# Kernel optimization log

Hardware: AMD Instinct MI355X
Metric: run time of the kernel (lower is better)

Reference implementation:

```python
import jax, jax.numpy as jnp
import numpy as np

NS, NV = 32, 8            # scalar / vector multiplicities
N_NODES, N_EDGES = 40000, 120000
HID = 3 * NS              # edge-feature / MLP hidden size
WNUM = NS*NS + NS*NV + NV*NV + NV*NS + NV*NV  # 1664 tp weights per edge


def setup_inputs() -> dict:
    key = jax.random.key(0)
    ks = jax.random.split(key, 8)
    return {
        'node_attr': jax.random.normal(ks[0], (N_NODES, NS + 3*NV), jnp.float32),
        'edge_attr': jax.random.normal(ks[1], (N_EDGES, HID), jnp.float32),
        'edge_sh':   jax.random.normal(ks[2], (N_EDGES, 4), jnp.float32),
        'W1': jax.random.normal(ks[3], (HID, HID), jnp.float32) / np.sqrt(HID),
        'b1': jnp.zeros((HID,), jnp.float32),
        'W2': jax.random.normal(ks[4], (HID, WNUM), jnp.float32) / np.sqrt(HID),
        'b2': jnp.zeros((WNUM,), jnp.float32),
        'edge_src': jax.random.randint(ks[5], (N_EDGES,), 0, N_NODES, jnp.int32),
        'edge_dst': jax.random.randint(ks[6], (N_EDGES,), 0, N_NODES, jnp.int32),
    }


def _tp_conv(node_attr, edge_attr, edge_sh, W1, b1, W2, b2, edge_src, edge_dst):
    E = edge_attr.shape[0]
    N = node_attr.shape[0]
    # --- gather destination node features per edge ---
    x = node_attr[edge_dst]                      # [E, NS+3*NV]
    x0 = x[:, :NS]                               # [E, NS]  0e scalars
    x1 = x[:, NS:].reshape(E, NV, 3)             # [E, NV, 3]  1o vectors
    s0 = edge_sh[:, 0]                           # [E]     sh 0e
    sh1 = edge_sh[:, 1:4]                        # [E, 3]  sh 1o
    # --- per-edge weight generation MLP ---
    h = jax.nn.relu(edge_attr @ W1 + b1)
    w = h @ W2 + b2                              # [E, WNUM]
    o = 0
    w1 = w[:, o:o+NS*NS].reshape(E, NS, NS); o += NS*NS   # 0e x 0e -> 0e
    w2 = w[:, o:o+NS*NV].reshape(E, NS, NV); o += NS*NV   # 0e x 1o -> 1o
    w3 = w[:, o:o+NV*NV].reshape(E, NV, NV); o += NV*NV   # 1o x 0e -> 1o
    w4 = w[:, o:o+NV*NS].reshape(E, NV, NS); o += NV*NS   # 1o x 1o -> 0e (dot)
    w5 = w[:, o:o+NV*NV].reshape(E, NV, NV)               # 1o x 1o -> 1e (cross)
    inv_s3 = 1.0 / np.sqrt(3.0).astype(np.float32)
    inv_s2 = 1.0 / np.sqrt(2.0).astype(np.float32)
    n0 = 1.0 / np.sqrt(NS + NV).astype(np.float32)        # fan-in norm, 0e out
    n1o = n0                                              # fan-in norm, 1o out
    n1e = 1.0 / np.sqrt(NV).astype(np.float32)            # fan-in norm, 1e out
    # --- fully connected tensor product (CG contraction per path) ---
    out0 = (jnp.einsum('eu,euv->ev', x0, w1) * s0[:, None]
            + jnp.einsum('eum,em,euv->ev', x1, sh1, w4) * inv_s3) * n0   # [E, NS]
    out1o = (jnp.einsum('eu,euv->ev', x0, w2)[:, :, None] * sh1[:, None, :]
             + jnp.einsum('eum,euv->evm', x1, w3) * s0[:, None, None]) * n1o  # [E,NV,3]
    cr = jnp.cross(x1, sh1[:, None, :])                                  # [E, NV, 3]
    out1e = jnp.einsum('eum,euv->evm', cr, w5) * (inv_s2 * n1e)          # [E, NV, 3]
    tp = jnp.concatenate([out0, out1o.reshape(E, -1), out1e.reshape(E, -1)], axis=-1)
    # --- scatter-mean to source nodes ---
    seg = jax.ops.segment_sum(tp, edge_src, num_segments=N)
    cnt = jax.ops.segment_sum(jnp.ones((E,), tp.dtype), edge_src, num_segments=N)
    return seg / jnp.maximum(cnt, 1.0)[:, None]            # [N, NS+6*NV]


def reference(node_attr, edge_attr, edge_sh, W1, b1, W2, b2, edge_src, edge_dst):
    return _tp_conv(node_attr, edge_attr, edge_sh, W1, b1, W2, b2, edge_src, edge_dst)
```

## Files before the change

kernel.cpp:

```cpp
#include <hip/hip_runtime.h>
#include <hip/hip_bf16.h>

typedef short short8 __attribute__((ext_vector_type(8)));
typedef float f32x4 __attribute__((ext_vector_type(4)));
typedef unsigned int uint2v __attribute__((ext_vector_type(2)));

#define HID 96
#define WNUM 1664
#define NA_DIM 56
#define OUT_DIM 80
#define EPB 64
#define NT_TOT 104
#define CHW 208
#define NCH 8
#define NTC 13
#define APAD 104

#define N0f 0.158113883f
#define INV_S3 0.5773502692f
#define C_OUT1E 0.25f

__device__ __forceinline__ unsigned short f2bf(float x) {
  unsigned u = __builtin_bit_cast(unsigned, x);
  u += 0x7FFFu + ((u >> 16) & 1u);
  return (unsigned short)(u >> 16);
}
__device__ __forceinline__ unsigned short f2bf_hw(float x) {
  __hip_bfloat16 b = __float2bfloat16(x);
  return __builtin_bit_cast(unsigned short, b);
}

#if __has_builtin(__builtin_amdgcn_fdot2_f32_bf16)
typedef __bf16 bf16x2 __attribute__((ext_vector_type(2)));
#define DOT2(acc, w, x) \
  acc = __builtin_amdgcn_fdot2_f32_bf16(__builtin_bit_cast(bf16x2, (unsigned)(w)), \
                                        __builtin_bit_cast(bf16x2, (unsigned)(x)), (acc), false)
#else
#define DOT2(acc, w, x) do { \
  unsigned _w = (w), _x = (x); \
  acc = fmaf(__builtin_bit_cast(float, _w << 16), __builtin_bit_cast(float, _x << 16), acc); \
  acc = fmaf(__builtin_bit_cast(float, _w & 0xFFFF0000u), __builtin_bit_cast(float, _x & 0xFFFF0000u), acc); \
} while (0)
#endif

__device__ __forceinline__ int perm_col(int J) {
  int c = J / CHW, l = J - (J / CHW) * CHW;
  if (l < 128) { int vp = l >> 5, u = l & 31; return u * 32 + 4 * c + vp; }
  if (l < 160) { int u = l - 128; return 1024 + u * 8 + c; }
  if (l < 168) { int u = l - 160; return 1280 + u * 8 + c; }
  if (l < 200) { int q = l - 168; int vp = q >> 3, u = q & 7; return 1344 + u * 32 + 4 * c + vp; }
  { int u = l - 200; return 1600 + u * 8 + c; }
}

__global__ __launch_bounds__(256) void hist_kernel(
    const int* __restrict__ edge_src, int* __restrict__ hist, int E) {
  int e = blockIdx.x * 256 + threadIdx.x;
  if (e < E) atomicAdd(&hist[edge_src[e]], 1);
}

__global__ __launch_bounds__(256) void scan1_kernel(
    const int* __restrict__ hist, int* __restrict__ excl,
    int* __restrict__ bsum, int n) {
  __shared__ int s[256];
  int t = threadIdx.x, i = blockIdx.x * 256 + t;
  int v = (i < n) ? hist[i] : 0;
  s[t] = v;
  __syncthreads();
  #pragma unroll
  for (int off = 1; off < 256; off <<= 1) {
    int tv = (t >= off) ? s[t - off] : 0;
    __syncthreads();
    s[t] += tv;
    __syncthreads();
  }
  if (i < n) excl[i] = s[t] - v;
  if (t == 255) bsum[blockIdx.x] = s[255];
}

__global__ __launch_bounds__(256) void scan2_kernel(int* __restrict__ bsum, int nb) {
  __shared__ int s[256];
  int t = threadIdx.x;
  int v = (t < nb) ? bsum[t] : 0;
  s[t] = v;
  __syncthreads();
  #pragma unroll
  for (int off = 1; off < 256; off <<= 1) {
    int tv = (t >= off) ? s[t - off] : 0;
    __syncthreads();
    s[t] += tv;
    __syncthreads();
  }
  if (t < nb) bsum[t] = s[t] - v;
}

__global__ __launch_bounds__(256) void scan3_kernel(
    const int* __restrict__ excl, const int* __restrict__ bsum,
    int* __restrict__ start, int* __restrict__ cur, int n) {
  int i = blockIdx.x * 256 + threadIdx.x;
  if (i < n) {
    int v = excl[i] + bsum[blockIdx.x];
    start[i] = v;
    cur[i] = v;
  }
}

__global__ __launch_bounds__(256) void scatter_kernel(
    const int* __restrict__ edge_src, int* __restrict__ cur,
    int* __restrict__ pos, int E) {
  int e = blockIdx.x * 256 + threadIdx.x;
  if (e < E) {
    pos[e] = atomicAdd(&cur[edge_src[e]], 1);
  }
}

__global__ __launch_bounds__(256) void prep_kernel(
    const float* __restrict__ W2, const float* __restrict__ W1,
    const float* __restrict__ b2, unsigned short* __restrict__ W2p,
    unsigned short* __restrict__ W1p, float* __restrict__ b2p,
    int* __restrict__ hist, int nhist)
{
  int gid = blockIdx.x * 256 + threadIdx.x;
  if (gid < nhist) hist[gid] = 0;
  const int NW2 = NT_TOT * 3 * 64;
  const int NW1 = 18 * 64;
  if (gid < NW2) {
    int tile = gid >> 6, ln = gid & 63;
    int nt = tile / 3, s = tile - nt * 3;
    int J = nt * 16 + (ln & 15);
    int jo = perm_col(J);
    int kbase = s * 32 + ((ln >> 4) << 3);
    #pragma unroll
    for (int j = 0; j < 8; ++j)
      W2p[(size_t)gid * 8 + j] = f2bf(W2[(kbase + j) * WNUM + jo]);
  } else if (gid < NW2 + NW1) {
    int g = gid - NW2;
    int tile = g >> 6, ln = g & 63;
    int nt = tile / 3, s = tile - nt * 3;
    int col = nt * 16 + (ln & 15);
    int kbase = s * 32 + ((ln >> 4) << 3);
    #pragma unroll
    for (int j = 0; j < 8; ++j)
      W1p[(size_t)g * 8 + j] = f2bf(W1[(kbase + j) * HID + col]);
  } else if (gid < NW2 + NW1 + WNUM) {
    int J = gid - (NW2 + NW1);
    b2p[J] = b2[perm_col(J)];
  }
}

__global__ __launch_bounds__(512, 2) void fused_mfma(
    const float* __restrict__ edge_attr, const unsigned short* __restrict__ W1p,
    const float* __restrict__ b1, const unsigned short* __restrict__ W2p,
    const float* __restrict__ b2p, const float* __restrict__ node_attr,
    const float* __restrict__ edge_sh, const int* __restrict__ edge_dst,
    const int* __restrict__ pos, float* __restrict__ tpg)
{
  __shared__ __align__(16) unsigned short ws[2][EPB][212];
  __shared__ __align__(8) unsigned short x0h[EPB][32];
  __shared__ __align__(8) unsigned short x1h[EPB][3][8];
  __shared__ __align__(8) unsigned short dsuh[EPB][8];
  __shared__ __align__(8) unsigned short crsh[EPB][3][8];
  __shared__ float x1s[EPB][3][8];
  __shared__ float sh1s[EPB][3];
  __shared__ float s0s[EPB];
  __shared__ int   dsts[EPB];
  __shared__ int   poss[EPB];

  unsigned short* As = (unsigned short*)ws;
  unsigned short* hB = As + EPB * APAD;

  const int tid = threadIdx.x;
  const int e0 = blockIdx.x * EPB;

  if (tid < EPB) {
    dsts[tid] = edge_dst[e0 + tid];
    s0s[tid] = edge_sh[(size_t)(e0 + tid) * 4];
    poss[tid] = pos[e0 + tid];
  }
  if (tid >= 128 && tid < 128 + EPB * 3) {
    int i = tid - 128, e = i / 3, m = i - e * 3;
    sh1s[e][m] = edge_sh[(size_t)(e0 + e) * 4 + 1 + m];
  }
  __syncthreads();

  for (int idx = tid; idx < EPB * NA_DIM; idx += 512) {
    int e = idx / NA_DIM, c = idx - e * NA_DIM;
    float v = node_attr[(size_t)dsts[e] * NA_DIM + c];
    if (c < 32) x0h[e][c] = f2bf_hw(v);
    else { int q = c - 32; x1s[e][q % 3][q / 3] = v; x1h[e][q % 3][q / 3] = f2bf_hw(v); }
  }
  for (int idx = tid; idx < EPB * (HID / 4); idx += 512) {
    int e = idx / (HID / 4), c4 = (idx - e * (HID / 4)) * 4;
    f32x4 v = *(const f32x4*)&edge_attr[(size_t)(e0 + e) * HID + c4];
    unsigned short* d = &As[e * APAD + c4];
    d[0] = f2bf_hw(v[0]); d[1] = f2bf_hw(v[1]); d[2] = f2bf_hw(v[2]); d[3] = f2bf_hw(v[3]);
  }
  __syncthreads();

  {
    int e = tid >> 3, u = tid & 7;
    float a0 = x1s[e][0][u], a1 = x1s[e][1][u], a2 = x1s[e][2][u];
    float b0 = sh1s[e][0], b1v = sh1s[e][1], b2v = sh1s[e][2];
    dsuh[e][u] = f2bf_hw(a0 * b0 + a1 * b1v + a2 * b2v);
    crsh[e][0][u] = f2bf_hw(a1 * b2v - a2 * b1v);
    crsh[e][1][u] = f2bf_hw(a2 * b0 - a0 * b2v);
    crsh[e][2][u] = f2bf_hw(a0 * b1v - a1 * b0);
  }

  const int ln = tid & 63, wv = tid >> 6;
  const int c16 = ln & 15, q4 = (ln >> 4) << 2, k8 = (ln >> 4) << 3;

  #pragma unroll
  for (int t = 0; t < 3; ++t) {
    int tt_ = wv * 3 + t;
    int mtile = tt_ / 6, ntile = tt_ - mtile * 6;
    short8 aA[3];
    #pragma unroll
    for (int s = 0; s < 3; ++s)
      aA[s] = *(const short8*)&As[(mtile * 16 + c16) * APAD + s * 32 + k8];
    f32x4 acc = {0.f, 0.f, 0.f, 0.f};
    #pragma unroll
    for (int s = 0; s < 3; ++s) {
      short8 bfr = *(const short8*)(W1p + ((size_t)(ntile * 3 + s) * 64 + ln) * 8);
      acc = __builtin_amdgcn_mfma_f32_16x16x32_bf16(aA[s], bfr, acc, 0, 0, 0);
    }
    float bb = b1[ntile * 16 + c16];
    #pragma unroll
    for (int r = 0; r < 4; ++r)
      hB[(mtile * 16 + q4 + r) * APAD + ntile * 16 + c16] = f2bf_hw(fmaxf(acc[r] + bb, 0.f));
  }
  __syncthreads();

  short8 af[4][3];
  #pragma unroll
  for (int mt = 0; mt < 4; ++mt)
    #pragma unroll
    for (int s = 0; s < 3; ++s)
      af[mt][s] = *(const short8*)&hB[(mt * 16 + c16) * APAD + s * 32 + k8];
  __syncthreads();

  const int e = tid >> 3, tt = tid & 7;
  uint2v x0r[8], aux0, aux1;
  if (tt < 7) {
    #pragma unroll
    for (int i = 0; i < 8; ++i) x0r[i] = *(const uint2v*)&x0h[e][i * 4];
    if (tt < 4) {
      aux0 = *(const uint2v*)&dsuh[e][0];
      aux1 = *(const uint2v*)&dsuh[e][4];
    } else {
      aux0 = *(const uint2v*)&x1h[e][tt - 4][0];
      aux1 = *(const uint2v*)&x1h[e][tt - 4][4];
    }
  } else {
    #pragma unroll
    for (int m = 0; m < 3; ++m) {
      x0r[2 * m]     = *(const uint2v*)&crsh[e][m][0];
      x0r[2 * m + 1] = *(const uint2v*)&crsh[e][m][4];
    }
  }

  const int l0t = wv * 16 + c16;
  const int pc0t = (l0t & 96) | ((l0t + ((l0t >> 5) << 2)) & 31);
  const unsigned short* w2a = W2p + ((size_t)(wv * 3) * 64 + ln) * 8;
  const unsigned short* w2b = W2p + ((size_t)((wv + 8) * 3) * 64 + ln) * 8;
  const size_t CSTRIDE = (size_t)NTC * 3 * 64 * 8;
  const bool has1 = wv < (NTC - 8);

  auto compute_chunk = [&](int cc, unsigned short (*wsd)[212]) {
    const size_t cb = (size_t)cc * CSTRIDE;
    {
      f32x4 acc[4];
      #pragma unroll
      for (int mt = 0; mt < 4; ++mt) acc[mt] = (f32x4){0.f, 0.f, 0.f, 0.f};
      #pragma unroll
      for (int s = 0; s < 3; ++s) {
        short8 bfr = *(const short8*)(w2a + cb + (size_t)s * 64 * 8);
        #pragma unroll
        for (int mt = 0; mt < 4; ++mt)
          acc[mt] = __builtin_amdgcn_mfma_f32_16x16x32_bf16(af[mt][s], bfr, acc[mt], 0, 0, 0);
      }
      float bias = b2p[cc * CHW + l0t];
      #pragma unroll
      for (int mt = 0; mt < 4; ++mt)
        #pragma unroll
        for (int r = 0; r < 4; ++r)
          wsd[mt * 16 + q4 + r][pc0t] = f2bf_hw(acc[mt][r] + bias);
    }
    if (has1) {
      f32x4 acc[4];
      #pragma unroll
      for (int mt = 0; mt < 4; ++mt) acc[mt] = (f32x4){0.f, 0.f, 0.f, 0.f};
      #pragma unroll
      for (int s = 0; s < 3; ++s) {
        short8 bfr = *(const short8*)(w2b + cb + (size_t)s * 64 * 8);
        #pragma unroll
        for (int mt = 0; mt < 4; ++mt)
          acc[mt] = __builtin_amdgcn_mfma_f32_16x16x32_bf16(af[mt][s], bfr, acc[mt], 0, 0, 0);
      }
      float bias = b2p[cc * CHW + 128 + l0t];
      #pragma unroll
      for (int mt = 0; mt < 4; ++mt)
        #pragma unroll
        for (int r = 0; r < 4; ++r)
          wsd[mt * 16 + q4 + r][128 + l0t] = f2bf_hw(acc[mt][r] + bias);
    }
  };

  compute_chunk(0, ws[0]);
  __syncthreads();

  const float s0 = s0s[e];
  float* tpr = tpg + (size_t)poss[e] * OUT_DIM;

  for (int ch = 0; ch < NCH; ++ch) {
    if (ch < NCH - 1) compute_chunk(ch + 1, ws[(ch + 1) & 1]);

    const unsigned short (*wsr)[212] = ws[ch & 1];
    if (tt < 4) {
      float sa = 0.f, sb = 0.f;
      #pragma unroll
      for (int u0 = 0; u0 < 32; u0 += 8) {
        int pu  = (u0 + (tt << 2)) & 31;
        int pu2 = (u0 + 4 + (tt << 2)) & 31;
        uint2v wq  = *(const uint2v*)&wsr[e][(tt << 5) + pu];
        uint2v wq2 = *(const uint2v*)&wsr[e][(tt << 5) + pu2];
        uint2v xq  = x0r[u0 >> 2];
        uint2v xq2 = x0r[(u0 >> 2) + 1];
        DOT2(sa, wq[0], xq[0]);
        DOT2(sa, wq[1], xq[1]);
        DOT2(sb, wq2[0], xq2[0]);
        DOT2(sb, wq2[1], xq2[1]);
      }
      float s2 = 0.f;
      {
        uint2v wq  = *(const uint2v*)&wsr[e][168 + (tt << 3)];
        uint2v wq2 = *(const uint2v*)&wsr[e][168 + (tt << 3) + 4];
        DOT2(s2, wq[0], aux0[0]);
        DOT2(s2, wq[1], aux0[1]);
        DOT2(s2, wq2[0], aux1[0]);
        DOT2(s2, wq2[1], aux1[1]);
      }
      tpr[4 * ch + tt] = N0f * (s0 * (sa + sb) + INV_S3 * s2);
    } else if (tt < 7) {
      const int m = tt - 4;
      float sa = 0.f, sb = 0.f;
      #pragma unroll
      for (int u0 = 0; u0 < 32; u0 += 8) {
        uint2v wq  = *(const uint2v*)&wsr[e][128 + u0];
        uint2v wq2 = *(const uint2v*)&wsr[e][128 + u0 + 4];
        uint2v xq  = x0r[u0 >> 2];
        uint2v xq2 = x0r[(u0 >> 2) + 1];
        DOT2(sa, wq[0], xq[0]);
        DOT2(sa, wq[1], xq[1]);
        DOT2(sb, wq2[0], xq2[0]);
        DOT2(sb, wq2[1], xq2[1]);
      }
      float s2 = 0.f;
      {
        uint2v wq  = *(const uint2v*)&wsr[e][160];
        uint2v wq2 = *(const uint2v*)&wsr[e][164];
        DOT2(s2, wq[0], aux0[0]);
        DOT2(s2, wq[1], aux0[1]);
        DOT2(s2, wq2[0], aux1[0]);
        DOT2(s2, wq2[1], aux1[1]);
      }
      tpr[32 + ch * 3 + m] = N0f * (sh1s[e][m] * (sa + sb) + s0 * s2);
    } else {
      #pragma unroll
      for (int m = 0; m < 3; ++m) {
        float s2 = 0.f;
        uint2v wq  = *(const uint2v*)&wsr[e][200];
        uint2v wq2 = *(const uint2v*)&wsr[e][204];
        DOT2(s2, wq[0], x0r[2 * m][0]);
        DOT2(s2, wq[1], x0r[2 * m][1]);
        DOT2(s2, wq2[0], x0r[2 * m + 1][0]);
        DOT2(s2, wq2[1], x0r[2 * m + 1][1]);
        tpr[56 + ch * 3 + m] = C_OUT1E * s2;
      }
    }
    __syncthreads();
  }
}

__global__ __launch_bounds__(256) void gather_kernel(
    const float* __restrict__ tp, const int* __restrict__ start,
    const int* __restrict__ hist, float* __restrict__ out, int total)
{
  int idx = blockIdx.x * 256 + threadIdx.x;
  if (idx >= total) return;
  int node = idx / OUT_DIM, o = idx - node * OUT_DIM;
  int s = start[node], c = hist[node];
  float sum = 0.f;
  for (int i = 0; i < c; ++i)
    sum += tp[(size_t)(s + i) * OUT_DIM + o];
  out[idx] = sum / (float)(c > 0 ? c : 1);
}

extern "C" void kernel_launch(void* const* d_in, const int* in_sizes, int n_in,
                              void* d_out, int out_size, void* d_ws, size_t ws_size,
                              hipStream_t stream) {
  const float* node_attr = (const float*)d_in[0];
  const float* edge_attr = (const float*)d_in[1];
  const float* edge_sh   = (const float*)d_in[2];
  const float* W1        = (const float*)d_in[3];
  const float* b1        = (const float*)d_in[4];
  const float* W2        = (const float*)d_in[5];
  const float* b2        = (const float*)d_in[6];
  const int*   edge_src  = (const int*)d_in[7];
  const int*   edge_dst  = (const int*)d_in[8];
  float* out = (float*)d_out;

  const int E = in_sizes[7];
  const int N = in_sizes[0] / NA_DIM;

  char* wsb = (char*)d_ws;
  int*   hist  = (int*)(wsb + 0x000000);
  int*   excl  = (int*)(wsb + 0x040000);
  int*   start = (int*)(wsb + 0x080000);
  int*   cur   = (int*)(wsb + 0x0C0000);
  int*   bsum  = (int*)(wsb + 0x100000);
  int*   pos   = (int*)(wsb + 0x110000);
  unsigned short* W2p = (unsigned short*)(wsb + 0x200000);
  unsigned short* W1p = (unsigned short*)(wsb + 0x280000);
  float*          b2p = (float*)(wsb + 0x2C0000);
  float*          tpg = (float*)(wsb + 0x1C00000);

  const int NB = (N + 255) / 256;

  const int prep_total = NT_TOT * 3 * 64 + 18 * 64 + WNUM;
  const int prep_grid = ((prep_total > N ? prep_total : N) + 255) / 256;
  prep_kernel<<<prep_grid, 256, 0, stream>>>(W2, W1, b2, W2p, W1p, b2p, hist, N);

  hist_kernel<<<(E + 255) / 256, 256, 0, stream>>>(edge_src, hist, E);
  scan1_kernel<<<NB, 256, 0, stream>>>(hist, excl, bsum, N);
  scan2_kernel<<<1, 256, 0, stream>>>(bsum, NB);
  scan3_kernel<<<NB, 256, 0, stream>>>(excl, bsum, start, cur, N);
  scatter_kernel<<<(E + 255) / 256, 256, 0, stream>>>(edge_src, cur, pos, E);

  fused_mfma<<<E / EPB, 512, 0, stream>>>(edge_attr, W1p, b1, W2p, b2p,
                                          node_attr, edge_sh, edge_dst, pos, tpg);
  gather_kernel<<<(N * OUT_DIM + 255) / 256, 256, 0, stream>>>(
      tpg, start, hist, out, N * OUT_DIM);
}
```

Baseline: 152.6 us.

## Merge scan kernels, fold scatter into fused kernel, store per-edge results in bf16

Folds the second and third scan passes into one kernel: every block redundantly scans the block sums and adds its own offset. The separate scatter kernel goes away, and the fused MFMA kernel now claims each edge's output slot itself with an atomicAdd on the node cursor. Per-edge tensor-product outputs are stored as bf16 instead of fp32, halving the intermediate buffer traffic read by the gather kernel. The dot-product accumulators are split into more independent chains. These changes cut two launches and memory traffic at the cost of extra rounding on the intermediate values and a nondeterministic slot order.

```diff
diff --git a/kernel.cpp b/kernel.cpp
--- a/kernel.cpp
+++ b/kernel.cpp
@@ -28,6 +28,10 @@
 __device__ __forceinline__ unsigned short f2bf_hw(float x) {
   __hip_bfloat16 b = __float2bfloat16(x);
   return __builtin_bit_cast(unsigned short, b);
+}
+__device__ __forceinline__ float bf2f(unsigned short x) {
+  unsigned u = ((unsigned)x) << 16;
+  return __builtin_bit_cast(float, u);
 }
 
 #if __has_builtin(__builtin_amdgcn_fdot2_f32_bf16)
@@ -77,7 +81,9 @@
   if (t == 255) bsum[blockIdx.x] = s[255];
 }
 
-__global__ __launch_bounds__(256) void scan2_kernel(int* __restrict__ bsum, int nb) {
+__global__ __launch_bounds__(256) void scan23_kernel(
+    const int* __restrict__ excl, const int* __restrict__ bsum,
+    int* __restrict__ start, int* __restrict__ cur, int n, int nb) {
   __shared__ int s[256];
   int t = threadIdx.x;
   int v = (t < nb) ? bsum[t] : 0;
@@ -90,26 +96,12 @@
     s[t] += tv;
     __syncthreads();
   }
-  if (t < nb) bsum[t] = s[t] - v;
-}
-
-__global__ __launch_bounds__(256) void scan3_kernel(
-    const int* __restrict__ excl, const int* __restrict__ bsum,
-    int* __restrict__ start, int* __restrict__ cur, int n) {
-  int i = blockIdx.x * 256 + threadIdx.x;
+  int add = (blockIdx.x > 0) ? s[blockIdx.x - 1] : 0;
+  int i = blockIdx.x * 256 + t;
   if (i < n) {
-    int v = excl[i] + bsum[blockIdx.x];
-    start[i] = v;
-    cur[i] = v;
-  }
-}
-
-__global__ __launch_bounds__(256) void scatter_kernel(
-    const int* __restrict__ edge_src, int* __restrict__ cur,
-    int* __restrict__ pos, int E) {
-  int e = blockIdx.x * 256 + threadIdx.x;
-  if (e < E) {
-    pos[e] = atomicAdd(&cur[edge_src[e]], 1);
+    int val = excl[i] + add;
+    start[i] = val;
+    cur[i] = val;
   }
 }
 
@@ -151,8 +143,9 @@
     const float* __restrict__ edge_attr, const unsigned short* __restrict__ W1p,
     const float* __restrict__ b1, const unsigned short* __restrict__ W2p,
     const float* __restrict__ b2p, const float* __restrict__ node_attr,
-    const float* __restrict__ edge_sh, const int* __restrict__ edge_dst,
-    const int* __restrict__ pos, float* __restrict__ tpg)
+    const float* __restrict__ edge_sh, const int* __restrict__ edge_src,
+    const int* __restrict__ edge_dst, int* __restrict__ cur,
+    unsigned short* __restrict__ tpg)
 {
   __shared__ __align__(16) unsigned short ws[2][EPB][212];
   __shared__ __align__(8) unsigned short x0h[EPB][32];
@@ -174,7 +167,7 @@
   if (tid < EPB) {
     dsts[tid] = edge_dst[e0 + tid];
     s0s[tid] = edge_sh[(size_t)(e0 + tid) * 4];
-    poss[tid] = pos[e0 + tid];
+    poss[tid] = atomicAdd(&cur[edge_src[e0 + tid]], 1);
   }
   if (tid >= 128 && tid < 128 + EPB * 3) {
     int i = tid - 128, e = i / 3, m = i - e * 3;
@@ -309,14 +302,14 @@
   __syncthreads();
 
   const float s0 = s0s[e];
-  float* tpr = tpg + (size_t)poss[e] * OUT_DIM;
+  unsigned short* tpr = tpg + (size_t)poss[e] * OUT_DIM;
 
   for (int ch = 0; ch < NCH; ++ch) {
     if (ch < NCH - 1) compute_chunk(ch + 1, ws[(ch + 1) & 1]);
 
     const unsigned short (*wsr)[212] = ws[ch & 1];
     if (tt < 4) {
-      float sa = 0.f, sb = 0.f;
+      float c0 = 0.f, c1 = 0.f, c2 = 0.f, c3 = 0.f;
       #pragma unroll
       for (int u0 = 0; u0 < 32; u0 += 8) {
         int pu  = (u0 + (tt << 2)) & 31;
@@ -325,56 +318,58 @@
         uint2v wq2 = *(const uint2v*)&wsr[e][(tt << 5) + pu2];
         uint2v xq  = x0r[u0 >> 2];
         uint2v xq2 = x0r[(u0 >> 2) + 1];
-        DOT2(sa, wq[0], xq[0]);
-        DOT2(sa, wq[1], xq[1]);
-        DOT2(sb, wq2[0], xq2[0]);
-        DOT2(sb, wq2[1], xq2[1]);
-      }
-      float s2 = 0.f;
+        DOT2(c0, wq[0], xq[0]);
+        DOT2(c1, wq[1], xq[1]);
+        DOT2(c2, wq2[0], xq2[0]);
+        DOT2(c3, wq2[1], xq2[1]);
+      }
+      float d0 = 0.f, d1 = 0.f;
       {
         uint2v wq  = *(const uint2v*)&wsr[e][168 + (tt << 3)];
         uint2v wq2 = *(const uint2v*)&wsr[e][168 + (tt << 3) + 4];
-        DOT2(s2, wq[0], aux0[0]);
-        DOT2(s2, wq[1], aux0[1]);
-        DOT2(s2, wq2[0], aux1[0]);
-        DOT2(s2, wq2[1], aux1[1]);
-      }
-      tpr[4 * ch + tt] = N0f * (s0 * (sa + sb) + INV_S3 * s2);
+        DOT2(d0, wq[0], aux0[0]);
+        DOT2(d1, wq[1], aux0[1]);
+        DOT2(d0, wq2[0], aux1[0]);
+        DOT2(d1, wq2[1], aux1[1]);
+      }
+      float sum1 = (c0 + c1) + (c2 + c3);
+      tpr[4 * ch + tt] = f2bf_hw(N0f * (s0 * sum1 + INV_S3 * (d0 + d1)));
     } else if (tt < 7) {
       const int m = tt - 4;
-      float sa = 0.f, sb = 0.f;
+      float c0 = 0.f, c1 = 0.f, c2 = 0.f, c3 = 0.f;
       #pragma unroll
       for (int u0 = 0; u0 < 32; u0 += 8) {
         uint2v wq  = *(const uint2v*)&wsr[e][128 + u0];
         uint2v wq2 = *(const uint2v*)&wsr[e][128 + u0 + 4];
         uint2v xq  = x0r[u0 >> 2];
         uint2v xq2 = x0r[(u0 >> 2) + 1];
-        DOT2(sa, wq[0], xq[0]);
-        DOT2(sa, wq[1], xq[1]);
-        DOT2(sb, wq2[0], xq2[0]);
-        DOT2(sb, wq2[1], xq2[1]);
-      }
-      float s2 = 0.f;
+        DOT2(c0, wq[0], xq[0]);
+        DOT2(c1, wq[1], xq[1]);
+        DOT2(c2, wq2[0], xq2[0]);
+        DOT2(c3, wq2[1], xq2[1]);
+      }
+      float d0 = 0.f, d1 = 0.f;
       {
         uint2v wq  = *(const uint2v*)&wsr[e][160];
         uint2v wq2 = *(const uint2v*)&wsr[e][164];
-        DOT2(s2, wq[0], aux0[0]);
-        DOT2(s2, wq[1], aux0[1]);
-        DOT2(s2, wq2[0], aux1[0]);
-        DOT2(s2, wq2[1], aux1[1]);
-      }
-      tpr[32 + ch * 3 + m] = N0f * (sh1s[e][m] * (sa + sb) + s0 * s2);
+        DOT2(d0, wq[0], aux0[0]);
+        DOT2(d1, wq[1], aux0[1]);
+        DOT2(d0, wq2[0], aux1[0]);
+        DOT2(d1, wq2[1], aux1[1]);
+      }
+      float sum1 = (c0 + c1) + (c2 + c3);
+      tpr[32 + ch * 3 + m] = f2bf_hw(N0f * (sh1s[e][m] * sum1 + s0 * (d0 + d1)));
     } else {
+      uint2v wq  = *(const uint2v*)&wsr[e][200];
+      uint2v wq2 = *(const uint2v*)&wsr[e][204];
       #pragma unroll
       for (int m = 0; m < 3; ++m) {
-        float s2 = 0.f;
-        uint2v wq  = *(const uint2v*)&wsr[e][200];
-        uint2v wq2 = *(const uint2v*)&wsr[e][204];
-        DOT2(s2, wq[0], x0r[2 * m][0]);
-        DOT2(s2, wq[1], x0r[2 * m][1]);
-        DOT2(s2, wq2[0], x0r[2 * m + 1][0]);
-        DOT2(s2, wq2[1], x0r[2 * m + 1][1]);
-        tpr[56 + ch * 3 + m] = C_OUT1E * s2;
+        float d0 = 0.f, d1 = 0.f;
+        DOT2(d0, wq[0], x0r[2 * m][0]);
+        DOT2(d1, wq[1], x0r[2 * m][1]);
+        DOT2(d0, wq2[0], x0r[2 * m + 1][0]);
+        DOT2(d1, wq2[1], x0r[2 * m + 1][1]);
+        tpr[56 + ch * 3 + m] = f2bf_hw(C_OUT1E * (d0 + d1));
       }
     }
     __syncthreads();
@@ -382,7 +377,7 @@
 }
 
 __global__ __launch_bounds__(256) void gather_kernel(
-    const float* __restrict__ tp, const int* __restrict__ start,
+    const unsigned short* __restrict__ tp, const int* __restrict__ start,
     const int* __restrict__ hist, float* __restrict__ out, int total)
 {
   int idx = blockIdx.x * 256 + threadIdx.x;
@@ -391,7 +386,7 @@
   int s = start[node], c = hist[node];
   float sum = 0.f;
   for (int i = 0; i < c; ++i)
-    sum += tp[(size_t)(s + i) * OUT_DIM + o];
+    sum += bf2f(tp[(size_t)(s + i) * OUT_DIM + o]);
   out[idx] = sum / (float)(c > 0 ? c : 1);
 }
 
@@ -418,11 +413,10 @@
   int*   start = (int*)(wsb + 0x080000);
   int*   cur   = (int*)(wsb + 0x0C0000);
   int*   bsum  = (int*)(wsb + 0x100000);
-  int*   pos   = (int*)(wsb + 0x110000);
   unsigned short* W2p = (unsigned short*)(wsb + 0x200000);
   unsigned short* W1p = (unsigned short*)(wsb + 0x280000);
   float*          b2p = (float*)(wsb + 0x2C0000);
-  float*          tpg = (float*)(wsb + 0x1C00000);
+  unsigned short* tpg = (unsigned short*)(wsb + 0x1C00000);
 
   const int NB = (N + 255) / 256;
 
@@ -432,12 +426,11 @@
 
   hist_kernel<<<(E + 255) / 256, 256, 0, stream>>>(edge_src, hist, E);
   scan1_kernel<<<NB, 256, 0, stream>>>(hist, excl, bsum, N);
-  scan2_kernel<<<1, 256, 0, stream>>>(bsum, NB);
-  scan3_kernel<<<NB, 256, 0, stream>>>(excl, bsum, start, cur, N);
-  scatter_kernel<<<(E + 255) / 256, 256, 0, stream>>>(edge_src, cur, pos, E);
+  scan23_kernel<<<NB, 256, 0, stream>>>(excl, bsum, start, cur, N, NB);
 
   fused_mfma<<<E / EPB, 512, 0, stream>>>(edge_attr, W1p, b1, W2p, b2p,
-                                          node_attr, edge_sh, edge_dst, pos, tpg);
+                                          node_attr, edge_sh, edge_src, edge_dst,
+                                          cur, tpg);
   gather_kernel<<<(N * OUT_DIM + 255) / 256, 256, 0, stream>>>(
       tpg, start, hist, out, N * OUT_DIM);
 }
```

Measured after the change: 148.2 us. -2.9%, faster.
